# Kernel optimization log

Hardware: AMD Instinct MI355X
Metric: run time of the kernel (lower is better)

Reference implementation:

```python
import jax, jax.numpy as jnp
import numpy as np

# Module hyperparameters (init_kwargs)
L_ORDER = 10
R_ORDER = 2
L_STRIDE = 1
R_STRIDE = 1
D_V = 512

# Input dims
B, H, T = 16, 4, 1024


def setup_inputs() -> dict:
    key = jax.random.key(0)
    k1, k2, k3 = jax.random.split(key, 3)
    v = jax.random.normal(k1, (B, H, T, D_V), dtype=jnp.float32)
    # torch uses randn init; scale by 0.05 so the IIR recurrence over T=1024
    # frames stays numerically stable (same math, just a sane parameter point).
    l_filter = jax.random.normal(k2, (L_ORDER, D_V), dtype=jnp.float32) * 0.05
    r_filter = jax.random.normal(k3, (R_ORDER, D_V), dtype=jnp.float32) * 0.05
    return {"v": v, "l_filter": l_filter, "r_filter": r_filter}


def dfsmn_forward(v, l_filter, r_filter):
    # Semantics of the torch in-place loop over frames t = 0..T-1:
    #   p[t] = v[t] + l_filter[0]*v[t]                       (k=0 tap reads pre-update p[t]=v[t])
    #        + sum_{k=1}^{L-1} l_filter[k] * p[t - k*ls]     (past frames: ALREADY updated -> IIR)
    #        + sum_{j=1}^{R}   r_filter[j-1] * v[t + j*rs]   (future frames: NOT yet updated -> read v)
    # out-of-range taps are dropped (the while loops break).
    Bv, Hv, Tv, D = v.shape

    # "base" = everything that does not depend on updated past frames (fully vectorized)
    base = v * (1.0 + l_filter[0])  # (B,H,T,D)
    vpad = jnp.pad(v, ((0, 0), (0, 0), (0, R_ORDER * R_STRIDE), (0, 0)))
    for j in range(1, R_ORDER + 1):  # tiny fixed loop over right taps
        base = base + r_filter[j - 1] * jax.lax.dynamic_slice_in_dim(
            vpad, j * R_STRIDE, Tv, axis=2)

    # IIR part: p[t] = base[t] + sum_{k=1}^{L-1} l_filter[k] * p[t - k*ls]
    Wn = (L_ORDER - 1) * L_STRIDE  # history window length
    tap_idx = np.array([k * L_STRIDE - 1 for k in range(1, L_ORDER)])  # buf[i] = p[t-1-i]
    lf = l_filter[1:]  # (L-1, D)

    base_t = jnp.moveaxis(base, 2, 0)  # (T,B,H,D)
    buf0 = jnp.zeros((Wn, Bv, Hv, D), dtype=v.dtype)  # zeros == dropped out-of-range taps

    def step(buf, b_t):
        taps = buf[tap_idx]  # (L-1,B,H,D)
        p_t = b_t + jnp.einsum('kd,kbhd->bhd', lf, taps)
        buf = jnp.concatenate([p_t[None], buf[:-1]], axis=0)
        return buf, p_t

    _, p = jax.lax.scan(step, buf0, base_t)  # p: (T,B,H,D)
    return jnp.moveaxis(p, 0, 2)  # (B,H,T,D)


def reference(v, l_filter, r_filter):
    return dfsmn_forward(v, l_filter, r_filter)
```

## Files before the change

kernel.cpp:

```cpp
#include <hip/hip_runtime.h>

#define BB 16
#define HH 4
#define TT 1024
#define DD 512
#define NTAP 9


#define DFSMN_BLOCK(CUR, NXT, TB, STORE)                                     \
  {                                                                          \
    _Pragma("unroll")                                                        \
    for (int u = 0; u < 32; ++u) {                                           \
      const int idx = (TB) + 34 + u;                                         \
      NXT[u] = (idx < TT) ? vp[(size_t)idx * DD] : 0.0f;                     \
    }                                                                        \
    _Pragma("unroll")                                                        \
    for (int u = 0; u < 32; ++u) {                                           \
      const float vt  = (u == 0) ? w0 : ((u == 1) ? w1 : CUR[(u < 2) ? 0 : (u - 2)]); \
      const float vt1 = (u == 0) ? w1 : CUR[(u < 1) ? 0 : (u - 1)];          \
      const float vt2 = CUR[u];                                              \
      float p = fmaf(vt, c0, r0 * vt1);                                      \
      p = fmaf(r1, vt2, p);                                                  \
                 \
      _Pragma("unroll")                                                      \
      for (int k = NTAP - 1; k >= 0; --k)                                    \
        p = fmaf(a[k], hist[(u + 15 - k) & 15], p);                          \
      hist[u & 15] = p;                                                      \
      if (STORE) __builtin_nontemporal_store(p, &op[(size_t)((TB) + u) * DD]); \
    }                                                                        \
    w0 = CUR[30];                                                            \
    w1 = CUR[31];                                                            \
  }

__global__ __launch_bounds__(128, 1) void dfsmn_kernel(
    const float* __restrict__ v,
    const float* __restrict__ lfilt,
    const float* __restrict__ rfilt,
    float* __restrict__ out)
{
    const int d  = blockIdx.x * 128 + threadIdx.x;
    const int bh = blockIdx.y;

    const float* __restrict__ vp = v + (size_t)bh * TT * DD + d;
    float* __restrict__ op = out + (size_t)bh * TT * DD + d;

    const float c0 = 1.0f + lfilt[d];
    float a[NTAP];
#pragma unroll
    for (int k = 0; k < NTAP; ++k) a[k] = lfilt[(k + 1) * DD + d];
    const float r0 = rfilt[d];
    const float r1 = rfilt[DD + d];

    float hist[16];
#pragma unroll
    for (int i = 0; i < 16; ++i) hist[i] = 0.0f;

    float A0[32], A1[32];
    float w0 = vp[0];
    float w1 = vp[(size_t)1 * DD];
#pragma unroll
    for (int u = 0; u < 32; ++u) {
        A0[u] = vp[(size_t)(2 + u) * DD];
    }

    for (int tb = 0; tb < TT; tb += 64) {
        DFSMN_BLOCK(A0, A1, tb, true)
        DFSMN_BLOCK(A1, A0, tb + 32, true)
    }
}

extern "C" void kernel_launch(void* const* d_in, const int* in_sizes, int n_in,
                              void* d_out, int out_size, void* d_ws, size_t ws_size,
                              hipStream_t stream) {
    const float* v  = (const float*)d_in[0];
    const float* lf = (const float*)d_in[1];
    const float* rf = (const float*)d_in[2];
    float* out = (float*)d_out;

    dim3 grid(DD / 128, BB * HH, 1);
    dim3 block(128, 1, 1);
    dfsmn_kernel<<<grid, block, 0, stream>>>(v, lf, rf, out);
}
```

Before: 52.71 us.

## Stream input tiles through LDS with async global_load_lds double buffering

Replaces per-thread register prefetch of future frames with asynchronous global-to-LDS DMA loads (16-byte vectorized per lane) into a double-buffered shared tile, synchronized through explicit vmcnt waits. Block size drops to a single 64-lane wave, so the grid holds twice as many blocks, and the right-tap window is now carried in two rolling registers. The aim is to cut register pressure and widen memory loads while overlapping them with the serial IIR compute. It depends on hand-counted vmcnt values and sched barriers being correct, and it zeros the tail LDS rows for out-of-range frames.

```diff
diff --git a/kernel.cpp b/kernel.cpp
--- a/kernel.cpp
+++ b/kernel.cpp
@@ -1,47 +1,63 @@
 #include <hip/hip_runtime.h>
+#include <stdint.h>
 
 #define BB 16
 #define HH 4
 #define TT 1024
 #define DD 512
 #define NTAP 9
+#define TS 32
 
 
-#define DFSMN_BLOCK(CUR, NXT, TB, STORE)                                     \
-  {                                                                          \
-    _Pragma("unroll")                                                        \
-    for (int u = 0; u < 32; ++u) {                                           \
-      const int idx = (TB) + 34 + u;                                         \
-      NXT[u] = (idx < TT) ? vp[(size_t)idx * DD] : 0.0f;                     \
+typedef __attribute__((address_space(3))) uint32_t lds_u32;
+typedef __attribute__((address_space(1))) const uint32_t glb_u32;
+
+#define WAITV(n) asm volatile("s_waitcnt vmcnt(" #n ")" ::: "memory")
+#define SB() __builtin_amdgcn_sched_barrier(0)
+
+#define ISSUE_TILE(LP, T0)                                                   \
+  { _Pragma("unroll")                                                        \
+    for (int i = 0; i < 8; ++i) {                                            \
+      int rr_ = (T0) + 4 * i + row_off;                                      \
+      rr_ = (rr_ < TT) ? rr_ : (TT - 1);                                     \
+      const float* gp_ = vrow + (size_t)rr_ * DD + col_off;                  \
+      __builtin_amdgcn_global_load_lds((glb_u32*)gp_,                        \
+                                       (lds_u32*)((LP) + i * 256),           \
+                                       16, 0, 0);                            \
     }                                                                        \
-    _Pragma("unroll")                                                        \
-    for (int u = 0; u < 32; ++u) {                                           \
-      const float vt  = (u == 0) ? w0 : ((u == 1) ? w1 : CUR[(u < 2) ? 0 : (u - 2)]); \
-      const float vt1 = (u == 0) ? w1 : CUR[(u < 1) ? 0 : (u - 1)];          \
-      const float vt2 = CUR[u];                                              \
-      float p = fmaf(vt, c0, r0 * vt1);                                      \
+    SB(); }
+
+#define COMPUTE_TILE(BUFI, TB)                                               \
+  { _Pragma("unroll")                                                        \
+    for (int u = 0; u < TS; ++u) {                                           \
+      const float vt2 = lds[BUFI][u * 64 + lane];                            \
+      float p = fmaf(w0, c0, r0 * w1);                                       \
       p = fmaf(r1, vt2, p);                                                  \
-                 \
       _Pragma("unroll")                                                      \
-      for (int k = NTAP - 1; k >= 0; --k)                                    \
-        p = fmaf(a[k], hist[(u + 15 - k) & 15], p);                          \
+      for (int kk = NTAP - 1; kk >= 0; --kk)                                 \
+        p = fmaf(a[kk], hist[(u + 15 - kk) & 15], p);                        \
       hist[u & 15] = p;                                                      \
-      if (STORE) __builtin_nontemporal_store(p, &op[(size_t)((TB) + u) * DD]); \
-    }                                                                        \
-    w0 = CUR[30];                                                            \
-    w1 = CUR[31];                                                            \
-  }
+      __builtin_nontemporal_store(p, &op[(size_t)((TB) + u) * DD]);          \
+      w0 = w1; w1 = vt2;                                                     \
+    } }
 
-__global__ __launch_bounds__(128, 1) void dfsmn_kernel(
+__global__ __launch_bounds__(64, 1) void dfsmn_kernel(
     const float* __restrict__ v,
     const float* __restrict__ lfilt,
     const float* __restrict__ rfilt,
     float* __restrict__ out)
 {
-    const int d  = blockIdx.x * 128 + threadIdx.x;
-    const int bh = blockIdx.y;
+    __shared__ float lds[2][TS * 64];
 
-    const float* __restrict__ vp = v + (size_t)bh * TT * DD + d;
+    const int lane = threadIdx.x;
+    const int dq   = blockIdx.x;
+    const int bh   = blockIdx.y;
+    const int d    = dq * 64 + lane;
+
+    const int row_off = lane >> 4;
+    const int col_off = (lane & 15) * 4;
+
+    const float* __restrict__ vrow = v + (size_t)bh * TT * DD + dq * 64;
     float* __restrict__ op = out + (size_t)bh * TT * DD + d;
 
     const float c0 = 1.0f + lfilt[d];
@@ -55,18 +71,37 @@
 #pragma unroll
     for (int i = 0; i < 16; ++i) hist[i] = 0.0f;
 
-    float A0[32], A1[32];
-    float w0 = vp[0];
-    float w1 = vp[(size_t)1 * DD];
-#pragma unroll
-    for (int u = 0; u < 32; ++u) {
-        A0[u] = vp[(size_t)(2 + u) * DD];
+    float w0 = vrow[lane];
+    float w1 = vrow[DD + lane];
+
+    ISSUE_TILE(lds[0], 2);
+    ISSUE_TILE(lds[1], 34);
+
+    WAITV(8); SB();
+    COMPUTE_TILE(0, 0);
+    ISSUE_TILE(lds[0], 66);
+
+#pragma unroll 1
+    for (int k = 1; k <= 27; k += 2) {
+        WAITV(40); SB();
+        COMPUTE_TILE(1, 32 * k);
+        ISSUE_TILE(lds[1], 32 * (k + 2) + 2);
+        WAITV(40); SB();
+        COMPUTE_TILE(0, 32 * (k + 1));
+        ISSUE_TILE(lds[0], 32 * (k + 3) + 2);
     }
 
-    for (int tb = 0; tb < TT; tb += 64) {
-        DFSMN_BLOCK(A0, A1, tb, true)
-        DFSMN_BLOCK(A1, A0, tb + 32, true)
-    }
+    WAITV(40); SB();
+    COMPUTE_TILE(1, 928);
+    ISSUE_TILE(lds[1], 994);
+
+    WAITV(40); SB();
+    COMPUTE_TILE(0, 960);
+
+    WAITV(32); SB();
+    lds[1][30 * 64 + lane] = 0.0f;
+    lds[1][31 * 64 + lane] = 0.0f;
+    COMPUTE_TILE(1, 992);
 }
 
 extern "C" void kernel_launch(void* const* d_in, const int* in_sizes, int n_in,
@@ -77,7 +112,7 @@
     const float* rf = (const float*)d_in[2];
     float* out = (float*)d_out;
 
-    dim3 grid(DD / 128, BB * HH, 1);
-    dim3 block(128, 1, 1);
+    dim3 grid(DD / 64, BB * HH, 1);
+    dim3 block(64, 1, 1);
     dfsmn_kernel<<<grid, block, 0, stream>>>(v, lf, rf, out);
 }
```

Result: faster. 45.54 us (-13.6%).
